# Kernel optimization log

Measured on AMD Instinct MI355X. Metric: run time of the kernel, lower is better.

Reference implementation:

```python
import jax, jax.numpy as jnp
import numpy as np

SC = 11  # window stride / block size; unfold kernel = 3*SC = 33, padding = SC


def _unfold3(x, sc):
    """Equivalent of nn.Unfold(kernel=3*sc, stride=sc, padding=sc) on [b,c,H,W]
    where H, W are multiples of sc. Returns [b, c, 9*sc*sc, n_windows].
    Patch ordering within K differs from torch by a fixed permutation, which is
    immaterial: all contractions over K (mask, softmax, value aggregation) are
    permutation-invariant as long as the same unfold is used everywhere."""
    b, c, H, W = x.shape
    h_sc, w_sc = H // sc, W // sc
    xp = jnp.pad(x, ((0, 0), (0, 0), (sc, sc), (sc, sc)))
    blk = xp.reshape(b, c, h_sc + 2, sc, w_sc + 2, sc)
    # 3x3 neighborhood of sc-blocks around each window
    pat = jnp.stack([blk[:, :, di:di + h_sc, :, dj:dj + w_sc, :]
                     for di in range(3) for dj in range(3)], axis=2)
    # [b,c,9,h_sc,r,w_sc,s] -> [b,c,9,r,s,h_sc,w_sc] -> [b,c,9*sc*sc,n]
    pat = pat.transpose(0, 1, 2, 4, 6, 3, 5)
    return pat.reshape(b, c, 9 * sc * sc, h_sc * w_sc)


def _block_q(x, sc):
    """view(b,c,h_sc,sc,w_sc,sc).permute(0,1,2,4,3,5) -> [b,c,n,sc*sc]"""
    b, c, H, W = x.shape
    h_sc, w_sc = H // sc, W // sc
    y = x.reshape(b, c, h_sc, sc, w_sc, sc).transpose(0, 1, 2, 4, 3, 5)
    return y.reshape(b, c, h_sc * w_sc, sc * sc)


def setup_inputs() -> dict:
    key = jax.random.key(0)
    k1, k2, k3, k4, k5, k6 = jax.random.split(key, 6)
    b, c, h, w = 2, 64, 256, 256
    s = 1.0 / np.sqrt(c)
    return {
        "x_key": jax.random.normal(k1, (b, c, h, w), jnp.float32),
        "x_ref": jax.random.normal(k2, (b, c, h, w), jnp.float32),
        "Wq": jax.random.normal(k3, (c, c), jnp.float32) * s,
        "Wk": jax.random.normal(k4, (c, c), jnp.float32) * s,
        "Wv": jax.random.normal(k5, (c, c), jnp.float32) * s,
        "gamma": jax.random.normal(k6, (1,), jnp.float32) * 0.1,
    }


def reference(x_key, x_ref, Wq, Wk, Wv, gamma):
    sc = SC
    b, c, h_in, w_in = x_key.shape
    x_pad = sc - w_in % sc
    y_pad = sc - h_in % sc
    pad = ((0, 0), (0, 0), (0, y_pad), (0, x_pad))
    fk = jnp.pad(x_key, pad)
    fr = jnp.pad(x_ref, pad)
    b, c, h, w = fk.shape
    h_sc, w_sc = h // sc, w // sc

    # validity mask -> additive attention bias (out-of-image keys penalized)
    fm = jnp.pad(jnp.ones((1, 1, h_in, w_in), fk.dtype), pad)
    fm_k = _unfold3(fm, sc)          # [1,1,K,n]
    fm_q = _block_q(fm, sc)          # [1,1,n,s]
    am = (jnp.einsum('bckn,bcns->bkns', fm_k, fm_q) - 1.0) * 99.0  # [1,K,n,s]

    scale = c ** (-0.5)
    q = jnp.einsum('oi,bihw->bohw', Wq, fk)
    k = jnp.einsum('oi,bihw->bohw', Wk, fr)
    v = jnp.einsum('oi,bihw->bohw', Wv, fr)

    k_u = _unfold3(k, sc) * scale    # [b,c,K,n]
    q_b = _block_q(q, sc)            # [b,c,n,s]
    attn = jnp.einsum('bckn,bcns->bkns', k_u, q_b) + am  # [b,K,n,s]
    attn = jax.nn.softmax(attn, axis=1)

    v_u = _unfold3(v, sc)            # [b,c,K,n]
    r = jnp.einsum('bkns,bckn->bcns', attn, v_u)  # [b,c,n,s]
    r = r.reshape(b, c, h_sc, w_sc, sc, sc).transpose(0, 1, 2, 4, 3, 5)
    r = r.reshape(b, c, h, w)[:, :, :h_in, :w_in]
    return x_ref + r * gamma[0]
```

## Files before the change

kernel.cpp:

```cpp
#include <hip/hip_runtime.h>


typedef unsigned short ushort_t;
typedef unsigned int   uint32;
typedef unsigned long long uint64;
typedef __attribute__((ext_vector_type(8))) short short8;
typedef __attribute__((ext_vector_type(4))) float f32x4;

#define MFMA16(a,b,c) __builtin_amdgcn_mfma_f32_16x16x32_bf16(a,b,c,0,0,0)

#if __has_builtin(__builtin_amdgcn_exp2f)
#define EXP2(x) __builtin_amdgcn_exp2f(x)
#else
#define EXP2(x) exp2f(x)
#endif
#if __has_builtin(__builtin_amdgcn_rcpf)
#define RCP(x) __builtin_amdgcn_rcpf(x)
#else
#define RCP(x) (1.0f/(x))
#endif

#define QPKT_OFF   0u
#define KPKT_OFF   18874368u
#define VPKT_OFF   37748736u

__device__ __forceinline__ ushort_t f2bf(float f){
  union { __bf16 h; ushort_t u; } c;
  c.h = (__bf16)f;
  return c.u;
}

__device__ __forceinline__ uint32 pkbf(float a, float b){
  union { __bf16 h[2]; uint32 u; } c;
  c.h[0] = (__bf16)a;
  c.h[1] = (__bf16)b;
  return c.u;
}

__device__ __forceinline__ void storeK8(ushort_t* __restrict__ base, int nt, int t,
                                        int l15, int h, f32x4 a){
  uint32 lo = pkbf(a[0], a[1]);
  uint32 hi = pkbf(a[2], a[3]);
  int lanep = l15 + 16*((2*t + (h>>1)) & 3);
  size_t off = (size_t)((nt*2 + (t>>1))*64 + lanep)*16 + 8*(h&1);
  *(uint2*)((char*)base + off) = make_uint2(lo, hi);
}

__device__ __forceinline__ short8 ldWfrag(const float* __restrict__ W, int t, int ks,
                                          int l15, int h, float scale){
  const float* p = W + (16*t + l15)*64 + 32*ks + 8*h;
  float4 a = *(const float4*)p;
  float4 b = *(const float4*)(p + 4);
  union { uint4 u; short8 s; } x;
  x.u.x = pkbf(a.x*scale, a.y*scale);
  x.u.y = pkbf(a.z*scale, a.w*scale);
  x.u.z = pkbf(b.x*scale, b.y*scale);
  x.u.w = pkbf(b.z*scale, b.w*scale);
  return x.s;
}

#define SXS 196
__global__ __launch_bounds__(256) void proj_kernel(
    const float* __restrict__ xk, const float* __restrict__ xr,
    const float* __restrict__ Wq, const float* __restrict__ Wk, const float* __restrict__ Wv,
    ushort_t* __restrict__ qpkt, ushort_t* __restrict__ kpkt, ushort_t* __restrict__ vpkt)
{
  __shared__ __align__(16) ushort_t sX[64*SXS];
  const int tid = threadIdx.x;
  const int lane = tid & 63, wv = tid >> 6;
  const int l15 = lane & 15, h = lane >> 4;
  const int bid = blockIdx.x;
  const bool isQ = bid >= 1152;
  const int id = isQ ? bid - 1152 : bid;
  const int b = id / 576, rem = id % 576, ty = rem / 24, tx = rem % 24;
  const float* xs = (isQ ? xk : xr) + (size_t)b*64*65536;
  const int oy = ty*11, ox = tx*11;
  const int ox3 = ox & 3, xa = ox - ox3;

  #pragma unroll
  for (int i = tid; i < 1024; i += 256) sX[(i>>4)*SXS + 176 + (i&15)] = 0;

  {
    const int ch = tid >> 2, seg = tid & 3;
    const float* rowp = xs + (size_t)ch*65536 + (size_t)oy*256 + (xa + 4*seg);
    ushort_t* sdst = sX + ch*SXS + 4*seg;
    if (ty < 23 && tx < 23){
      #pragma unroll
      for (int y = 0; y < 11; ++y){
        float4 v = *(const float4*)(rowp + y*256);
        *(uint2*)(sdst + y*16) = make_uint2(pkbf(v.x, v.y), pkbf(v.z, v.w));
      }
    } else {
      const int xg = xa + 4*seg;
      #pragma unroll
      for (int y = 0; y < 11; ++y){
        const bool rk = (oy + y) < 256;
        float4 v;
        v.x = (rk && xg+0 < 256) ? rowp[y*256+0] : 0.f;
        v.y = (rk && xg+1 < 256) ? rowp[y*256+1] : 0.f;
        v.z = (rk && xg+2 < 256) ? rowp[y*256+2] : 0.f;
        v.w = (rk && xg+3 < 256) ? rowp[y*256+3] : 0.f;
        *(uint2*)(sdst + y*16) = make_uint2(pkbf(v.x, v.y), pkbf(v.z, v.w));
      }
    }
  }
  __syncthreads();

  const f32x4 zero = {0.f, 0.f, 0.f, 0.f};
  #define XFL(nt, ks, dst) { \
    const int px_ = 16*(nt) + l15; \
    const int y_ = (px_*745) >> 13; \
    const ushort_t* pp_ = sX + (32*(ks) + 8*h)*SXS + y_*16 + (px_ - y_*11) + ox3; \
    union { uint4 u; short8 s; } r_; \
    r_.u.x = (uint32)pp_[0*SXS] | ((uint32)pp_[1*SXS] << 16); \
    r_.u.y = (uint32)pp_[2*SXS] | ((uint32)pp_[3*SXS] << 16); \
    r_.u.z = (uint32)pp_[4*SXS] | ((uint32)pp_[5*SXS] << 16); \
    r_.u.w = (uint32)pp_[6*SXS] | ((uint32)pp_[7*SXS] << 16); \
    dst = r_.s; }

  if (!isQ){
    ushort_t* kb = kpkt + (size_t)id*8192;
    ushort_t* vb = vpkt + (size_t)id*8192;
    const int nt0 = 2*wv, nt1 = 2*wv + 1;
    short8 xf0[2], xf1[2];
    XFL(nt0, 0, xf0[0]); XFL(nt0, 1, xf0[1]);
    XFL(nt1, 0, xf1[0]); XFL(nt1, 1, xf1[1]);
    #pragma unroll
    for (int t = 0; t < 4; ++t){
      short8 wk0 = ldWfrag(Wk, t, 0, l15, h, 1.f), wk1 = ldWfrag(Wk, t, 1, l15, h, 1.f);
      short8 wv0 = ldWfrag(Wv, t, 0, l15, h, 1.f), wv1 = ldWfrag(Wv, t, 1, l15, h, 1.f);
      f32x4 ak0 = MFMA16(wk0, xf0[0], zero); ak0 = MFMA16(wk1, xf0[1], ak0);
      f32x4 ak1 = MFMA16(wk0, xf1[0], zero); ak1 = MFMA16(wk1, xf1[1], ak1);
      f32x4 av0 = MFMA16(xf0[0], wv0, zero); av0 = MFMA16(xf0[1], wv1, av0);
      f32x4 av1 = MFMA16(xf1[0], wv0, zero); av1 = MFMA16(xf1[1], wv1, av1);
      storeK8(kb, nt0, t, l15, h, ak0);
      storeK8(kb, nt1, t, l15, h, ak1);
      uint4 pv;
      pv.x = pkbf(av0[0], av0[1]); pv.y = pkbf(av0[2], av0[3]);
      pv.z = pkbf(av1[0], av1[1]); pv.w = pkbf(av1[2], av1[3]);
      *(uint4*)((char*)vb + (size_t)((wv*4 + t)*64 + lane)*16) = pv;
    }
  } else {
    const float C1 = 0.18033688011112042f;
    ushort_t* qb = qpkt + (size_t)id*8192;
    short8 xf[2][2];
    XFL(2*wv + 0, 0, xf[0][0]); XFL(2*wv + 0, 1, xf[0][1]);
    XFL(2*wv + 1, 0, xf[1][0]); XFL(2*wv + 1, 1, xf[1][1]);
    #pragma unroll
    for (int t = 0; t < 4; ++t){
      short8 wq0 = ldWfrag(Wq, t, 0, l15, h, C1), wq1 = ldWfrag(Wq, t, 1, l15, h, C1);
      #pragma unroll
      for (int nn = 0; nn < 2; ++nn){
        f32x4 aq = MFMA16(wq0, xf[nn][0], zero); aq = MFMA16(wq1, xf[nn][1], aq);
        storeK8(qb, 2*wv + nn, t, l15, h, aq);
      }
    }
  }
  #undef XFL
}
#undef SXS

__global__ __launch_bounds__(256) void attn_kernel(
    ushort_t* qpkt,
    const ushort_t* __restrict__ kpkt, const ushort_t* __restrict__ vpkt,
    const float* __restrict__ gamma)
{
  __shared__ __align__(16) char smem[49152];
  const int tid = threadIdx.x;
  const int lane = tid & 63, wave = tid >> 6;
  const int qh = wave & 1, kh = wave >> 1;
  const int win = (blockIdx.x & 7)*144 + (blockIdx.x >> 3);
  const int b = win / 576, wid = win % 576, wy = wid / 24, wx = wid % 24;
  const int l15 = lane & 15, h = lane >> 4;

  short8 qf[4][2];
  {
    const ushort_t* qblk = qpkt + (size_t)win*8192;
    #pragma unroll
    for (int mt = 0; mt < 4; ++mt){
      qf[mt][0] = *(const short8*)(qblk + (size_t)(((4*qh+mt)*2 + 0)*64 + lane)*8);
      qf[mt][1] = *(const short8*)(qblk + (size_t)(((4*qh+mt)*2 + 1)*64 + lane)*8);
    }
  }

  uint64 cks = 0; int nv = 0;
  #pragma unroll
  for (int ck = 0; ck < 9; ++ck){
    const int ty = wy - 1 + ck/3, tx = wx - 1 + ck%3;
    if ((unsigned)ty < 24u && (unsigned)tx < 24u){
      cks |= ((uint64)ck) << (4*nv); ++nv;
    }
  }
  const int nu = 2*nv;

  const f32x4 zz = {0.f,0.f,0.f,0.f};
  f32x4 o[4][4], lsumC[4];
  #pragma unroll
  for (int mt = 0; mt < 4; ++mt){
    lsumC[mt] = zz;
    #pragma unroll
    for (int u = 0; u < 4; ++u) o[mt][u] = zz;
  }
  f32x4 init_i;
  #pragma unroll
  for (int r = 0; r < 4; ++r) init_i[r] = (4*h + r >= 9) ? -1.0e4f : 0.f;
  short8 ones;
  #pragma unroll
  for (int j = 0; j < 8; ++j) ones[j] = (short)0x3F80;

  const ushort_t* gsrc = (wave < 2) ? kpkt : vpkt;
  const int ldsoff = (wave >> 1)*8192 + (wave & 1)*4096;

  #define STAGE(u, bo) { \
    const int t_ = (u) >> 1, hf_ = (u) & 1; \
    const int ck_ = (int)((cks >> (4*t_)) & 15); \
    const int cy_ = (ck_*11) >> 5; \
    const int ty_ = wy - 1 + cy_, tx_ = wx - 1 + (ck_ - 3*cy_); \
    const char* g_ = (const char*)(gsrc + (size_t)(b*576 + ty_*24 + tx_)*8192) \
                     + hf_*8192 + (wave & 1)*4096 + lane*16; \
    char* l_ = smem + (bo)*16384 + ldsoff + lane*16; \
    _Pragma("unroll") \
    for (int i_ = 0; i_ < 4; ++i_) \
      __builtin_amdgcn_global_load_lds( \
        (const __attribute__((address_space(1))) uint32*)(g_ + i_*1024), \
        (__attribute__((address_space(3))) uint32*)(l_ + i_*1024), 16, 0, 0); \
  }

  STAGE(0, 0);
  STAGE(1, 1);

  int bu = 0;
  #pragma unroll 1
  for (int u = 0; u < nu; ++u){
    if (u + 1 < nu) { __asm__ volatile("s_waitcnt vmcnt(4)" ::: "memory"); }
    else            { __asm__ volatile("s_waitcnt vmcnt(0)" ::: "memory"); }
    __builtin_amdgcn_s_barrier();
    __asm__ volatile("" ::: "memory");

    const int bn = (bu == 2) ? 0 : bu + 1;
    const int b2 = (bn == 2) ? 0 : bn + 1;
    if (u + 2 < nu) STAGE(u + 2, b2);

    const int t = u >> 1, hf = u & 1;
    const int ckv = (int)((cks >> (4*t)) & 15);
    const int cyv = (ckv*11) >> 5;
    const int tyv = wy - 1 + cyv, txv = wx - 1 + (ckv - 3*cyv);
    const bool ey = (tyv == 23), ex = (txv == 23);
    const int ntp = 2*hf + kh;

    f32x4 b0, b1;
    if (ey | ex){
      #pragma unroll
      for (int kt = 0; kt < 2; ++kt){
        f32x4 bb;
        #pragma unroll
        for (int r = 0; r < 4; ++r){
          const int kl = 32*ntp + 16*kt + 4*h + r;
          const int ky = (kl*745) >> 13, kx = kl - ky*11;
          bool ok = (kl < 121) && (!ey || ky < 3) && (!ex || kx < 3);
          bb[r] = ok ? 0.f : -1.0e4f;
        }
        if (kt) b1 = bb; else b0 = bb;
      }
    } else {
      b0 = zz;
      b1 = (hf & kh) ? init_i : zz;
    }

    const char* lk = smem + bu*16384 + kh*4096;
    const char* lv = smem + bu*16384 + 8192 + kh*4096;
    short8 kf00 = *(const short8*)(lk + (0*64 + lane)*16);
    short8 kf01 = *(const short8*)(lk + (1*64 + lane)*16);
    short8 kf10 = *(const short8*)(lk + (2*64 + lane)*16);
    short8 kf11 = *(const short8*)(lk + (3*64 + lane)*16);
    short8 vf0  = *(const short8*)(lv + (0*64 + lane)*16);
    short8 vf1  = *(const short8*)(lv + (1*64 + lane)*16);
    short8 vf2  = *(const short8*)(lv + (2*64 + lane)*16);
    short8 vf3  = *(const short8*)(lv + (3*64 + lane)*16);

    __builtin_amdgcn_s_setprio(1);
    #pragma unroll
    for (int mt = 0; mt < 4; ++mt){
      f32x4 s0 = MFMA16(kf00, qf[mt][0], b0); s0 = MFMA16(kf01, qf[mt][1], s0);
      f32x4 s1 = MFMA16(kf10, qf[mt][0], b1); s1 = MFMA16(kf11, qf[mt][1], s1);
      float p[8];
      #pragma unroll
      for (int r = 0; r < 4; ++r){
        p[r]   = EXP2(s0[r]);
        p[4+r] = EXP2(s1[r]);
      }
      union { uint4 uu; short8 s; } af;
      af.uu.x = pkbf(p[0], p[1]); af.uu.y = pkbf(p[2], p[3]);
      af.uu.z = pkbf(p[4], p[5]); af.uu.w = pkbf(p[6], p[7]);
      o[mt][0] = MFMA16(af.s, vf0, o[mt][0]);
      o[mt][1] = MFMA16(af.s, vf1, o[mt][1]);
      o[mt][2] = MFMA16(af.s, vf2, o[mt][2]);
      o[mt][3] = MFMA16(af.s, vf3, o[mt][3]);
      lsumC[mt] = MFMA16(af.s, ones, lsumC[mt]);
    }
    __builtin_amdgcn_s_setprio(0);

    bu = bn;
  }
  #undef STAGE

  __syncthreads();
  {
    float* base = (float*)(smem + qh*12288);
    if (kh){
      #pragma unroll
      for (int mt = 0; mt < 4; ++mt){
        *(f32x4*)(base + (mt*2+0)*256 + lane*4) = o[mt][0];
        *(f32x4*)(base + (mt*2+1)*256 + lane*4) = o[mt][1];
        *(f32x4*)(base + (8+mt)*256 + lane*4)   = lsumC[mt];
      }
    }
  }
  __syncthreads();
  if (!kh){
    float* base = (float*)(smem + qh*12288);
    #pragma unroll
    for (int mt = 0; mt < 4; ++mt){
      o[mt][0] += *(const f32x4*)(base + (mt*2+0)*256 + lane*4);
      o[mt][1] += *(const f32x4*)(base + (mt*2+1)*256 + lane*4);
      lsumC[mt] += *(const f32x4*)(base + (8+mt)*256 + lane*4);
    }
  }
  __syncthreads();
  {
    float* base2 = (float*)(smem + qh*8192);
    if (kh){
      #pragma unroll
      for (int mt = 0; mt < 4; ++mt){
        *(f32x4*)(base2 + (mt*2+0)*256 + lane*4) = o[mt][2];
        *(f32x4*)(base2 + (mt*2+1)*256 + lane*4) = o[mt][3];
      }
    }
  }
  __syncthreads();
  if (!kh){
    float* base2 = (float*)(smem + qh*8192);
    #pragma unroll
    for (int mt = 0; mt < 4; ++mt){
      o[mt][2] += *(const f32x4*)(base2 + (mt*2+0)*256 + lane*4);
      o[mt][3] += *(const f32x4*)(base2 + (mt*2+1)*256 + lane*4);
    }
    const float gm = gamma[0];
    ushort_t* rb = qpkt + (size_t)win*8192 + (size_t)qh*4096;
    #pragma unroll
    for (int mt = 0; mt < 4; ++mt){
      #pragma unroll
      for (int r = 0; r < 4; ++r){
        const float wg = gm * RCP(lsumC[mt][r]);
        const int qs = 16*mt + 4*h + r;
        #pragma unroll
        for (int u = 0; u < 4; ++u)
          rb[(size_t)qs*64 + 16*u + l15] = f2bf(wg * o[mt][u][r]);
      }
    }
  }
}

__global__ __launch_bounds__(256) void ep_kernel(
    const float* __restrict__ xref, const ushort_t* __restrict__ rbuf,
    float* __restrict__ out)
{
  __shared__ float tile[64][65];
  const int tid = threadIdx.x;
  const int bidx = blockIdx.x;
  const int xc = bidx & 3, y = (bidx >> 2) & 255, b = bidx >> 10;
  const int wy = (y*745) >> 13, qy = y - wy*11;
  {
    const int ch2 = tid & 31;
    const int xg  = tid >> 5;
    #pragma unroll
    for (int xi = 0; xi < 8; ++xi){
      const int xl = xi*8 + xg;
      const int x = xc*64 + xl;
      const int wx = (x*745) >> 13, qx = x - wx*11;
      const size_t ridx = (size_t)(b*576 + wy*24 + wx)*8192 + (size_t)(qy*11 + qx)*64;
      const uint32 v = *(const uint32*)(rbuf + ridx + 2*ch2);
      tile[xl][2*ch2]     = __uint_as_float(v << 16);
      tile[xl][2*ch2 + 1] = __uint_as_float(v & 0xFFFF0000u);
    }
  }
  __syncthreads();
  {
    const int lr = tid & 15;
    const int cg = tid >> 4;
    const size_t base = (size_t)b*4194304 + (size_t)y*256 + xc*64 + 4*lr;
    #pragma unroll
    for (int ci = 0; ci < 4; ++ci){
      const int c2 = cg + 16*ci;
      const size_t idx = base + (size_t)c2*65536;
      float4 xv = *(const float4*)(xref + idx);
      float4 ov;
      ov.x = xv.x + tile[4*lr + 0][c2];
      ov.y = xv.y + tile[4*lr + 1][c2];
      ov.z = xv.z + tile[4*lr + 2][c2];
      ov.w = xv.w + tile[4*lr + 3][c2];
      *(float4*)(out + idx) = ov;
    }
  }
}

extern "C" void kernel_launch(void* const* d_in, const int* in_sizes, int n_in,
                              void* d_out, int out_size, void* d_ws, size_t ws_size,
                              hipStream_t stream)
{
  const float* xk = (const float*)d_in[0];
  const float* xr = (const float*)d_in[1];
  const float* Wq = (const float*)d_in[2];
  const float* Wk = (const float*)d_in[3];
  const float* Wv = (const float*)d_in[4];
  const float* gm = (const float*)d_in[5];
  float* out = (float*)d_out;
  char* ws = (char*)d_ws;
  ushort_t* qp = (ushort_t*)(ws + QPKT_OFF);
  ushort_t* kp = (ushort_t*)(ws + KPKT_OFF);
  ushort_t* vp = (ushort_t*)(ws + VPKT_OFF);
  (void)in_sizes; (void)n_in; (void)out_size; (void)ws_size;

  proj_kernel<<<2304, 256, 0, stream>>>(xk, xr, Wq, Wk, Wv, qp, kp, vp);
  attn_kernel<<<1152, 256, 0, stream>>>(qp, kp, vp, gm);
  ep_kernel<<<2048, 256, 0, stream>>>(xr, qp, out);
}
```

Measured before the change: 236.7 us.

## Stage projection input tiles via direct global-to-LDS loads and prefetch weights

For interior tiles, the projection kernel now loads the input tile with global_load_lds straight into shared memory as fp32 in a [row][channel][16] layout, instead of going through registers and converting to bf16 on the way in. The bf16 conversion moves to the LDS fragment reads. Weight fragments are loaded into registers before the barrier so their latency overlaps the async tile load. The cost is twice the LDS footprint (fp32 instead of bf16), more conversion work at fragment-build time, a possible change in LDS bank-conflict patterns, and higher register pressure from holding the weights.

```diff
diff --git a/kernel.cpp b/kernel.cpp
--- a/kernel.cpp
+++ b/kernel.cpp
@@ -59,13 +59,12 @@
   return x.s;
 }
 
-#define SXS 196
 __global__ __launch_bounds__(256) void proj_kernel(
     const float* __restrict__ xk, const float* __restrict__ xr,
     const float* __restrict__ Wq, const float* __restrict__ Wk, const float* __restrict__ Wv,
     ushort_t* __restrict__ qpkt, ushort_t* __restrict__ kpkt, ushort_t* __restrict__ vpkt)
 {
-  __shared__ __align__(16) ushort_t sX[64*SXS];
+  __shared__ __align__(16) float sX[12*64*16];
   const int tid = threadIdx.x;
   const int lane = tid & 63, wv = tid >> 6;
   const int l15 = lane & 15, h = lane >> 4;
@@ -78,44 +77,62 @@
   const int ox3 = ox & 3, xa = ox - ox3;
 
   #pragma unroll
-  for (int i = tid; i < 1024; i += 256) sX[(i>>4)*SXS + 176 + (i&15)] = 0;
-
-  {
+  for (int i = tid; i < 1024; i += 256) sX[11*1024 + i] = 0.f;
+
+  const bool interior = (ty < 23) && (tx < 23);
+  if (interior){
+    const int ch = 16*wv + (lane >> 2), seg = lane & 3;
+    const float* g0 = xs + (size_t)ch*65536 + (size_t)oy*256 + (xa + 4*seg);
+    char* l0 = (char*)sX + (size_t)(16*wv)*64 + (size_t)lane*16;
+    #pragma unroll
+    for (int y = 0; y < 11; ++y)
+      __builtin_amdgcn_global_load_lds(
+        (const __attribute__((address_space(1))) uint32*)(g0 + y*256),
+        (__attribute__((address_space(3))) uint32*)(l0 + y*4096), 16, 0, 0);
+  } else {
     const int ch = tid >> 2, seg = tid & 3;
     const float* rowp = xs + (size_t)ch*65536 + (size_t)oy*256 + (xa + 4*seg);
-    ushort_t* sdst = sX + ch*SXS + 4*seg;
-    if (ty < 23 && tx < 23){
-      #pragma unroll
-      for (int y = 0; y < 11; ++y){
-        float4 v = *(const float4*)(rowp + y*256);
-        *(uint2*)(sdst + y*16) = make_uint2(pkbf(v.x, v.y), pkbf(v.z, v.w));
-      }
-    } else {
-      const int xg = xa + 4*seg;
-      #pragma unroll
-      for (int y = 0; y < 11; ++y){
-        const bool rk = (oy + y) < 256;
-        float4 v;
-        v.x = (rk && xg+0 < 256) ? rowp[y*256+0] : 0.f;
-        v.y = (rk && xg+1 < 256) ? rowp[y*256+1] : 0.f;
-        v.z = (rk && xg+2 < 256) ? rowp[y*256+2] : 0.f;
-        v.w = (rk && xg+3 < 256) ? rowp[y*256+3] : 0.f;
-        *(uint2*)(sdst + y*16) = make_uint2(pkbf(v.x, v.y), pkbf(v.z, v.w));
-      }
-    }
-  }
-  __syncthreads();
+    const int xg = xa + 4*seg;
+    #pragma unroll
+    for (int y = 0; y < 11; ++y){
+      const bool rk = (oy + y) < 256;
+      float4 v;
+      v.x = (rk && xg+0 < 256) ? rowp[y*256+0] : 0.f;
+      v.y = (rk && xg+1 < 256) ? rowp[y*256+1] : 0.f;
+      v.z = (rk && xg+2 < 256) ? rowp[y*256+2] : 0.f;
+      v.w = (rk && xg+3 < 256) ? rowp[y*256+3] : 0.f;
+      *(float4*)(sX + (size_t)(y*64 + ch)*16 + 4*seg) = v;
+    }
+  }
 
   const f32x4 zero = {0.f, 0.f, 0.f, 0.f};
+  short8 wa[4][2], wb[4][2];
+  if (!isQ){
+    #pragma unroll
+    for (int t = 0; t < 4; ++t){
+      wa[t][0] = ldWfrag(Wk, t, 0, l15, h, 1.f);  wa[t][1] = ldWfrag(Wk, t, 1, l15, h, 1.f);
+      wb[t][0] = ldWfrag(Wv, t, 0, l15, h, 1.f);  wb[t][1] = ldWfrag(Wv, t, 1, l15, h, 1.f);
+    }
+  } else {
+    const float C1 = 0.18033688011112042f;
+    #pragma unroll
+    for (int t = 0; t < 4; ++t){
+      wa[t][0] = ldWfrag(Wq, t, 0, l15, h, C1);  wa[t][1] = ldWfrag(Wq, t, 1, l15, h, C1);
+    }
+  }
+
+  __asm__ volatile("s_waitcnt vmcnt(0)" ::: "memory");
+  __syncthreads();
+
   #define XFL(nt, ks, dst) { \
     const int px_ = 16*(nt) + l15; \
     const int y_ = (px_*745) >> 13; \
-    const ushort_t* pp_ = sX + (32*(ks) + 8*h)*SXS + y_*16 + (px_ - y_*11) + ox3; \
+    const float* pp_ = sX + (size_t)(y_*64 + 32*(ks) + 8*h)*16 + (px_ - y_*11) + ox3; \
     union { uint4 u; short8 s; } r_; \
-    r_.u.x = (uint32)pp_[0*SXS] | ((uint32)pp_[1*SXS] << 16); \
-    r_.u.y = (uint32)pp_[2*SXS] | ((uint32)pp_[3*SXS] << 16); \
-    r_.u.z = (uint32)pp_[4*SXS] | ((uint32)pp_[5*SXS] << 16); \
-    r_.u.w = (uint32)pp_[6*SXS] | ((uint32)pp_[7*SXS] << 16); \
+    r_.u.x = pkbf(pp_[0],   pp_[16]); \
+    r_.u.y = pkbf(pp_[32],  pp_[48]); \
+    r_.u.z = pkbf(pp_[64],  pp_[80]); \
+    r_.u.w = pkbf(pp_[96],  pp_[112]); \
     dst = r_.s; }
 
   if (!isQ){
@@ -127,12 +144,10 @@
     XFL(nt1, 0, xf1[0]); XFL(nt1, 1, xf1[1]);
     #pragma unroll
     for (int t = 0; t < 4; ++t){
-      short8 wk0 = ldWfrag(Wk, t, 0, l15, h, 1.f), wk1 = ldWfrag(Wk, t, 1, l15, h, 1.f);
-      short8 wv0 = ldWfrag(Wv, t, 0, l15, h, 1.f), wv1 = ldWfrag(Wv, t, 1, l15, h, 1.f);
-      f32x4 ak0 = MFMA16(wk0, xf0[0], zero); ak0 = MFMA16(wk1, xf0[1], ak0);
-      f32x4 ak1 = MFMA16(wk0, xf1[0], zero); ak1 = MFMA16(wk1, xf1[1], ak1);
-      f32x4 av0 = MFMA16(xf0[0], wv0, zero); av0 = MFMA16(xf0[1], wv1, av0);
-      f32x4 av1 = MFMA16(xf1[0], wv0, zero); av1 = MFMA16(xf1[1], wv1, av1);
+      f32x4 ak0 = MFMA16(wa[t][0], xf0[0], zero); ak0 = MFMA16(wa[t][1], xf0[1], ak0);
+      f32x4 ak1 = MFMA16(wa[t][0], xf1[0], zero); ak1 = MFMA16(wa[t][1], xf1[1], ak1);
+      f32x4 av0 = MFMA16(xf0[0], wb[t][0], zero); av0 = MFMA16(xf0[1], wb[t][1], av0);
+      f32x4 av1 = MFMA16(xf1[0], wb[t][0], zero); av1 = MFMA16(xf1[1], wb[t][1], av1);
       storeK8(kb, nt0, t, l15, h, ak0);
       storeK8(kb, nt1, t, l15, h, ak1);
       uint4 pv;
@@ -141,24 +156,21 @@
       *(uint4*)((char*)vb + (size_t)((wv*4 + t)*64 + lane)*16) = pv;
     }
   } else {
-    const float C1 = 0.18033688011112042f;
     ushort_t* qb = qpkt + (size_t)id*8192;
     short8 xf[2][2];
     XFL(2*wv + 0, 0, xf[0][0]); XFL(2*wv + 0, 1, xf[0][1]);
     XFL(2*wv + 1, 0, xf[1][0]); XFL(2*wv + 1, 1, xf[1][1]);
     #pragma unroll
     for (int t = 0; t < 4; ++t){
-      short8 wq0 = ldWfrag(Wq, t, 0, l15, h, C1), wq1 = ldWfrag(Wq, t, 1, l15, h, C1);
       #pragma unroll
       for (int nn = 0; nn < 2; ++nn){
-        f32x4 aq = MFMA16(wq0, xf[nn][0], zero); aq = MFMA16(wq1, xf[nn][1], aq);
+        f32x4 aq = MFMA16(wa[t][0], xf[nn][0], zero); aq = MFMA16(wa[t][1], xf[nn][1], aq);
         storeK8(qb, 2*wv + nn, t, l15, h, aq);
       }
     }
   }
   #undef XFL
 }
-#undef SXS
 
 __global__ __launch_bounds__(256) void attn_kernel(
     ushort_t* qpkt,
```

Result: no change. 235.8 us (-0.4%).
